# Kernel tuning notes

Hardware: AMD Instinct MI355X
Metric: run time of the kernel (lower is better)

The kernel has to match this reference:

```python
import jax, jax.numpy as jnp
import numpy as np

B, S, H = 8, 1024, 1536          # batch, seq, hidden_size
NH, HD, AH = 8, 96, 768          # heads after head_ratio=2, head_size=hidden/16, all_head_size
K = 7                            # conv_kernel_size
IM = 3072                        # intermediate_size
EPS = 1e-12                      # ConvBert layer_norm_eps


def _ln(x, g, b):
    m = x.mean(-1, keepdims=True)
    v = ((x - m) ** 2).mean(-1, keepdims=True)
    return (x - m) / jnp.sqrt(v + EPS) * g + b


def _windows(x, k):
    # x: [B,S,C] -> sliding windows [B,S,k,C] with 'same' padding ((k-1)//2 each side, k odd)
    p = (k - 1) // 2
    xp = jnp.pad(x, ((0, 0), (p, p), (0, 0)))
    idx = jnp.arange(x.shape[1])[:, None] + jnp.arange(k)[None, :]
    return xp[:, idx, :]


def _forward(embed, wq, bq, wk, bk, wv, bv, dw, pw, sep_b, wck, bck, wco, bco,
             wso, bso, ln1_g, ln1_b, wi, bi, wo, bo, ln2_g, ln2_b, wd, bd):
    b, s, _ = embed.shape
    # --- projections (weights stored [in,out]) ---
    q = embed @ wq + bq            # [B,S,AH]
    kk = embed @ wk + bk
    v = embed @ wv + bv
    # --- SeparableConv1D on hidden states: depthwise(k=7) then pointwise + bias ---
    win_h = _windows(embed, K)                             # [B,S,K,H]
    dconv = jnp.einsum('bskc,ck->bsc', win_h, dw)          # depthwise, [B,S,H]
    sep = dconv @ pw + sep_b                               # pointwise, [B,S,AH]
    # --- span dynamic conv kernels ---
    conv_attn = sep * q                                    # [B,S,AH]
    ck = (conv_attn @ wck + bck).reshape(b, s, NH, K)      # [B,S,NH,K]
    ck = jax.nn.softmax(ck, axis=-1)
    co = embed @ wco + bco                                 # [B,S,AH]
    win_co = _windows(co, K).reshape(b, s, K, NH, HD)      # [B,S,K,NH,HD]
    conv_out = jnp.einsum('bskhd,bshk->bshd', win_co, ck)  # [B,S,NH,HD]
    # --- standard self-attention on the reduced heads ---
    qh = q.reshape(b, s, NH, HD)
    kh = kk.reshape(b, s, NH, HD)
    vh = v.reshape(b, s, NH, HD)
    scores = jnp.einsum('bqhd,bkhd->bhqk', qh, kh) / jnp.sqrt(jnp.float32(HD))
    probs = jax.nn.softmax(scores, axis=-1)
    ctx = jnp.einsum('bhqk,bkhd->bqhd', probs, vh)         # [B,S,NH,HD]
    # --- concat attention heads with conv heads -> [B,S,2*NH,HD] -> [B,S,H] ---
    ctx = jnp.concatenate([ctx, conv_out], axis=2).reshape(b, s, H)
    # --- self output (dropout is identity at inference) ---
    attn_out = _ln(ctx @ wso + bso + embed, ln1_g, ln1_b)
    # --- FFN ---
    inter = jax.nn.gelu(attn_out @ wi + bi, approximate=False)
    layer_out = _ln(inter @ wo + bo + attn_out, ln2_g, ln2_b)
    # --- global max pooling over sequence + linear decoder ---
    pooled = layer_out.max(axis=1)                         # [B,H]
    logits = pooled @ wd + bd                              # [B,1]
    return logits


def setup_inputs() -> dict:
    key = jax.random.key(0)
    ks = jax.random.split(key, 32)
    rn = lambda i, shape, s=0.02: jax.random.normal(ks[i], shape, jnp.float32) * s
    d = {}
    d['embed'] = jax.random.normal(ks[0], (B, S, H), jnp.float32)
    d['wq'] = rn(1, (H, AH)); d['bq'] = jnp.zeros((AH,), jnp.float32)
    d['wk'] = rn(2, (H, AH)); d['bk'] = jnp.zeros((AH,), jnp.float32)
    d['wv'] = rn(3, (H, AH)); d['bv'] = jnp.zeros((AH,), jnp.float32)
    d['dw'] = rn(4, (H, K)); d['pw'] = rn(5, (H, AH)); d['sep_b'] = jnp.zeros((AH,), jnp.float32)
    d['wck'] = rn(6, (AH, NH * K)); d['bck'] = jnp.zeros((NH * K,), jnp.float32)
    d['wco'] = rn(7, (H, AH)); d['bco'] = jnp.zeros((AH,), jnp.float32)
    d['wso'] = rn(8, (H, H)); d['bso'] = jnp.zeros((H,), jnp.float32)
    d['ln1_g'] = jnp.ones((H,), jnp.float32); d['ln1_b'] = jnp.zeros((H,), jnp.float32)
    d['wi'] = rn(9, (H, IM)); d['bi'] = jnp.zeros((IM,), jnp.float32)
    d['wo'] = rn(10, (IM, H)); d['bo'] = jnp.zeros((H,), jnp.float32)
    d['ln2_g'] = jnp.ones((H,), jnp.float32); d['ln2_b'] = jnp.zeros((H,), jnp.float32)
    d['wd'] = jax.random.uniform(ks[11], (H, 1), jnp.float32, -0.1, 0.1)
    d['bd'] = jnp.zeros((1,), jnp.float32)
    return d


def reference(embed, wq, bq, wk, bk, wv, bv, dw, pw, sep_b, wck, bck, wco, bco,
              wso, bso, ln1_g, ln1_b, wi, bi, wo, bo, ln2_g, ln2_b, wd, bd):
    return _forward(embed, wq, bq, wk, bk, wv, bv, dw, pw, sep_b, wck, bck, wco, bco,
                    wso, bso, ln1_g, ln1_b, wi, bi, wo, bo, ln2_g, ln2_b, wd, bd)
```

## Files before the change

### kernel.cpp

```cpp
#include <hip/hip_runtime.h>


typedef __bf16 bf16_t;
typedef short s16x8 __attribute__((ext_vector_type(8)));
typedef float f32x4 __attribute__((ext_vector_type(4)));

#define BB  8
#define SS  1024
#define HH  1536
#define NHH 8
#define HDD 96
#define AHH 768
#define IMM 3072

__device__ __forceinline__ float rd_adapt(const void* p, long long i, int isbf) {
    return isbf ? (float)((const bf16_t*)p)[i] : ((const float*)p)[i];
}
__device__ __forceinline__ float bs2f(short x) {
    return __uint_as_float(((unsigned)(unsigned short)x) << 16);
}
__device__ __forceinline__ short f2bs(float f) {
    bf16_t b = (bf16_t)f; short s; __builtin_memcpy(&s, &b, 2); return s;
}

__device__ __forceinline__ float gelu_f(float v) {
    float u = v * (0.7978845608f + 0.0356774081f * v * v);
    float e = __expf(2.0f * u);
    float t = 1.0f - 2.0f / (e + 1.0f);
    return 0.5f * v * (1.0f + t);
}

__device__ __forceinline__ void gl2lds16(const bf16_t* g, bf16_t* l) {
    __builtin_amdgcn_global_load_lds(
        (__attribute__((address_space(1))) const void*)g,
        (__attribute__((address_space(3))) void*)l, 16, 0, 0);
}

#define FENCE() asm volatile("" ::: "memory")
#define BARRIER() do { FENCE(); __builtin_amdgcn_s_barrier(); FENCE(); } while (0)
#define LGKM(n) asm volatile("s_waitcnt lgkmcnt(" #n ")" ::: "memory")
#define VMCNT(n) asm volatile("s_waitcnt vmcnt(" #n ")" ::: "memory")
#define SCHEDB() __builtin_amdgcn_sched_barrier(0)
#define PRIO(n) __builtin_amdgcn_s_setprio(n)
#define RDV(base, imm) (*(const s16x8*)(smb + (base) + (imm)))

#define MFMA_CLUSTER(AF, BF, IO, JO)                                            \
    _Pragma("unroll")                                                           \
    for (int i_ = 0; i_ < 4; i_++)                                              \
        _Pragma("unroll")                                                       \
        for (int j_ = 0; j_ < 2; j_++) {                                        \
            acc[(IO)+i_][(JO)+j_] = __builtin_amdgcn_mfma_f32_16x16x32_bf16(    \
                AF[i_][0], BF[j_][0], acc[(IO)+i_][(JO)+j_], 0, 0, 0);          \
            acc[(IO)+i_][(JO)+j_] = __builtin_amdgcn_mfma_f32_16x16x32_bf16(    \
                AF[i_][1], BF[j_][1], acc[(IO)+i_][(JO)+j_], 0, 0, 0);          \
        }

__global__ __launch_bounds__(256)
void detect_kernel(const void* __restrict__ embed, int* __restrict__ flag)
{
    __shared__ int cnt[256];
    int t = threadIdx.x;
    float x = (float)((const bf16_t*)embed)[t];
    float a = fabsf(x);
    cnt[t] = (a > 1e-3f && a < 50.0f) ? 1 : 0;
    __syncthreads();
    for (int o = 128; o > 0; o >>= 1) { if (t < o) cnt[t] += cnt[t + o]; __syncthreads(); }
    if (t == 0) *flag = (cnt[0] >= 205) ? 1 : 0;
}

__global__ __launch_bounds__(256)
void convert_embed(const void* __restrict__ in, bf16_t* __restrict__ out,
                   const int* __restrict__ flagp)
{
    int isbf = *flagp;
    long long i0 = ((long long)blockIdx.x * 256 + threadIdx.x) * 8;
    if (isbf) {
        *(s16x8*)(out + i0) = *(const s16x8*)((const bf16_t*)in + i0);
    } else {
        const float* f = (const float*)in;
        #pragma unroll
        for (int j = 0; j < 8; j++) out[i0 + j] = (bf16_t)f[i0 + j];
    }
}

__global__ __launch_bounds__(256)
void concat_bias(const void* __restrict__ b0, const void* __restrict__ b1,
                 const void* __restrict__ b2, const void* __restrict__ b3,
                 bf16_t* __restrict__ out, const int* __restrict__ flagp)
{
    int isbf = *flagp;
    int t = blockIdx.x * 256 + threadIdx.x;
    int sel = t / 768, off = t - sel * 768;
    const void* src = (sel == 0) ? b0 : (sel == 1) ? b1 : (sel == 2) ? b2 : b3;
    out[t] = (bf16_t)rd_adapt(src, off, isbf);
}

__global__ __launch_bounds__(256)
void dw_transpose(const void* __restrict__ dw, float* __restrict__ dwT,
                  const int* __restrict__ flagp)
{
    int isbf = *flagp;
    int i = blockIdx.x * 256 + threadIdx.x;
    if (i >= 7 * HH) return;
    int k = i % 7, c = i / 7;
    dwT[k * HH + c] = rd_adapt(dw, (long long)c * 7 + k, isbf);
}

template<int IB, int OB>
__device__ __forceinline__ void tile_step(
    char* smb, int vA0, int vA1, int vB0, int vB1,
    const char* gA00, const char* gA01, const char* gA10, const char* gA11,
    const char* gB00, const char* gB01, const char* gB10, const char* gB11,
    char* ldsAw, char* ldsBw, int k1, int k2,
    s16x8 (&af0)[4][2], s16x8 (&af1)[4][2],
    s16x8 (&bf0)[2][2], s16x8 (&bf1)[2][2],
    f32x4 (&acc)[8][4])
{
    BARRIER();
    bf1[0][0] = RDV(vB0, IB + 4096); bf1[0][1] = RDV(vB1, IB + 4096);
    bf1[1][0] = RDV(vB0, IB + 6144); bf1[1][1] = RDV(vB1, IB + 6144);
    gl2lds16((const bf16_t*)(gA10 + k1), (bf16_t*)(ldsAw + OB + 16384));
    gl2lds16((const bf16_t*)(gA11 + k1), (bf16_t*)(ldsAw + OB + 17408));
    LGKM(4); SCHEDB(); PRIO(1);
    MFMA_CLUSTER(af0, bf0, 0, 0);
    PRIO(0);

    BARRIER();
    af1[0][0] = RDV(vA0, IB + 8192);  af1[0][1] = RDV(vA1, IB + 8192);
    af1[1][0] = RDV(vA0, IB + 10240); af1[1][1] = RDV(vA1, IB + 10240);
    af1[2][0] = RDV(vA0, IB + 12288); af1[2][1] = RDV(vA1, IB + 12288);
    af1[3][0] = RDV(vA0, IB + 14336); af1[3][1] = RDV(vA1, IB + 14336);
    gl2lds16((const bf16_t*)(gB10 + k1), (bf16_t*)(ldsBw + OB + 16384));
    gl2lds16((const bf16_t*)(gB11 + k1), (bf16_t*)(ldsBw + OB + 17408));
    LGKM(8); SCHEDB(); PRIO(1);
    MFMA_CLUSTER(af0, bf1, 0, 2);
    PRIO(0);

    BARRIER();
    gl2lds16((const bf16_t*)(gB00 + k2), (bf16_t*)(ldsBw + IB));
    gl2lds16((const bf16_t*)(gB01 + k2), (bf16_t*)(ldsBw + IB + 1024));
    gl2lds16((const bf16_t*)(gA00 + k2), (bf16_t*)(ldsAw + IB));
    gl2lds16((const bf16_t*)(gA01 + k2), (bf16_t*)(ldsAw + IB + 1024));
    LGKM(0); SCHEDB(); PRIO(1);
    MFMA_CLUSTER(af1, bf1, 4, 2);
    PRIO(0);

    VMCNT(4);
    BARRIER();
    af0[0][0] = RDV(vA0, OB + 0);    af0[0][1] = RDV(vA1, OB + 0);
    af0[1][0] = RDV(vA0, OB + 2048); af0[1][1] = RDV(vA1, OB + 2048);
    af0[2][0] = RDV(vA0, OB + 4096); af0[2][1] = RDV(vA1, OB + 4096);
    af0[3][0] = RDV(vA0, OB + 6144); af0[3][1] = RDV(vA1, OB + 6144);
    PRIO(1);
    MFMA_CLUSTER(af1, bf0, 4, 0);
    PRIO(0);
    bf0[0][0] = RDV(vB0, OB + 0);    bf0[0][1] = RDV(vB1, OB + 0);
    bf0[1][0] = RDV(vB0, OB + 2048); bf0[1][1] = RDV(vB1, OB + 2048);
}

__global__ __launch_bounds__(512, 2)
void gemm256(const bf16_t* __restrict__ A, const bf16_t* __restrict__ Bt,
             bf16_t* __restrict__ C, const void* __restrict__ bias,
             const bf16_t* __restrict__ emul, int lde, const int* __restrict__ flagp,
             int M, int N, int Kd, int lda, int ldb, int ldc, int act, int tilesN)
{
    __shared__ bf16_t Sm[65536];
    char* smb = (char*)Sm;
    int isbf = flagp ? *flagp : 1;

    int nwg = gridDim.x;
    int orig = blockIdx.x;
    int q = nwg >> 3, r = nwg & 7;
    int xcd = orig & 7, lid = orig >> 3;
    int wg = (xcd < r ? xcd * (q + 1) : r * (q + 1) + (xcd - r) * q) + lid;
    int row0 = (wg / tilesN) * 256;
    int col0 = (wg % tilesN) * 256;

    int tid = threadIdx.x;
    int wave = tid >> 6, lane = tid & 63;
    int wm = wave >> 2, wn = wave & 3;
    int lm = lane & 15, kq = lane >> 4;

    int srow = lane >> 3;
    int scol = 8 * ((lane & 7) ^ srow);

    const char* gA00 = (const char*)(A + (long long)(row0 +   0 + (2*wave + 0)*8 + srow) * lda + scol);
    const char* gA01 = (const char*)(A + (long long)(row0 +   0 + (2*wave + 1)*8 + srow) * lda + scol);
    const char* gA10 = (const char*)(A + (long long)(row0 + 128 + (2*wave + 0)*8 + srow) * lda + scol);
    const char* gA11 = (const char*)(A + (long long)(row0 + 128 + (2*wave + 1)*8 + srow) * lda + scol);
    const char* gB00 = (const char*)(Bt + (long long)(col0 +   0 + (2*wave + 0)*8 + srow) * ldb + scol);
    const char* gB01 = (const char*)(Bt + (long long)(col0 +   0 + (2*wave + 1)*8 + srow) * ldb + scol);
    const char* gB10 = (const char*)(Bt + (long long)(col0 + 128 + (2*wave + 0)*8 + srow) * ldb + scol);
    const char* gB11 = (const char*)(Bt + (long long)(col0 + 128 + (2*wave + 1)*8 + srow) * ldb + scol);

    char* ldsAw = smb + 2 * wave * 1024;
    char* ldsBw = smb + 65536 + 2 * wave * 1024;

    int xo = (lm & 7) << 4;
    int c0 = (kq * 16) ^ xo;
    int c1 = (64 + kq * 16) ^ xo;
    int vA0 = (wm * 128 + lm) * 128 + c0;
    int vA1 = (wm * 128 + lm) * 128 + c1;
    int vB0 = 65536 + (wn * 64 + lm) * 128 + c0;
    int vB1 = 65536 + (wn * 64 + lm) * 128 + c1;

    f32x4 acc[8][4] = {};
    s16x8 af0[4][2], af1[4][2], bf0[2][2], bf1[2][2];

    int KT = Kd >> 6;
    int KTm1 = KT - 1;

    gl2lds16((const bf16_t*)gA00, (bf16_t*)(ldsAw));
    gl2lds16((const bf16_t*)gA01, (bf16_t*)(ldsAw + 1024));
    gl2lds16((const bf16_t*)gA10, (bf16_t*)(ldsAw + 16384));
    gl2lds16((const bf16_t*)gA11, (bf16_t*)(ldsAw + 17408));
    gl2lds16((const bf16_t*)gB00, (bf16_t*)(ldsBw));
    gl2lds16((const bf16_t*)gB01, (bf16_t*)(ldsBw + 1024));
    gl2lds16((const bf16_t*)gB10, (bf16_t*)(ldsBw + 16384));
    gl2lds16((const bf16_t*)gB11, (bf16_t*)(ldsBw + 17408));
    int kb1 = min(1, KTm1) << 7;
    gl2lds16((const bf16_t*)(gB00 + kb1), (bf16_t*)(ldsBw + 32768));
    gl2lds16((const bf16_t*)(gB01 + kb1), (bf16_t*)(ldsBw + 33792));
    gl2lds16((const bf16_t*)(gA00 + kb1), (bf16_t*)(ldsAw + 32768));
    gl2lds16((const bf16_t*)(gA01 + kb1), (bf16_t*)(ldsAw + 33792));
    VMCNT(4);
    BARRIER();
    af0[0][0] = RDV(vA0, 0);    af0[0][1] = RDV(vA1, 0);
    af0[1][0] = RDV(vA0, 2048); af0[1][1] = RDV(vA1, 2048);
    af0[2][0] = RDV(vA0, 4096); af0[2][1] = RDV(vA1, 4096);
    af0[3][0] = RDV(vA0, 6144); af0[3][1] = RDV(vA1, 6144);
    bf0[0][0] = RDV(vB0, 0);    bf0[0][1] = RDV(vB1, 0);
    bf0[1][0] = RDV(vB0, 2048); bf0[1][1] = RDV(vB1, 2048);

    for (int it = 0; it < (KT >> 1); ++it) {
        int t = it << 1;
        int k1 = min(t + 1, KTm1) << 7;
        int k2 = min(t + 2, KTm1) << 7;
        int k3 = min(t + 3, KTm1) << 7;
        tile_step<0, 32768>(smb, vA0, vA1, vB0, vB1,
                            gA00, gA01, gA10, gA11, gB00, gB01, gB10, gB11,
                            ldsAw, ldsBw, k1, k2, af0, af1, bf0, bf1, acc);
        tile_step<32768, 0>(smb, vA0, vA1, vB0, vB1,
                            gA00, gA01, gA10, gA11, gB00, gB01, gB10, gB11,
                            ldsAw, ldsBw, k2, k3, af0, af1, bf0, bf1, acc);
    }

    #pragma unroll
    for (int j = 0; j < 4; j++) {
        int gcol = col0 + wn * 64 + j * 16 + lm;
        float bv = bias ? rd_adapt(bias, gcol, isbf) : 0.0f;
        #pragma unroll
        for (int ip = 0; ip < 8; ip++) {
            int grow0 = row0 + wm * 128 + ip * 16 + kq * 4;
            #pragma unroll
            for (int r = 0; r < 4; r++) {
                float v = acc[ip][j][r] + bv;
                if (emul) v *= (float)emul[(long long)(grow0 + r) * lde + gcol];
                if (act) v = gelu_f(v);
                C[(long long)(grow0 + r) * ldc + gcol] = (bf16_t)v;
            }
        }
    }
}

__global__ __launch_bounds__(256)
void gemm_tile(const bf16_t* __restrict__ A, const bf16_t* __restrict__ Bt,
               bf16_t* __restrict__ C, const void* __restrict__ bias, long long biasOff,
               const bf16_t* __restrict__ emul, int lde, const int* __restrict__ flagp,
               int M, int N, int Kd, int lda, int ldb, int ldc,
               float scale, int act, int beta, int nlim)
{
    __shared__ bf16_t Sm[16384];

    int isbf = flagp ? *flagp : 1;
    int tid  = threadIdx.x;
    int wave = tid >> 6, lane = tid & 63;
    int wm = wave >> 1, wn = wave & 1;
    int row0 = blockIdx.x * 128;
    int col0 = blockIdx.y * 128;
    int lm = lane & 15;
    int kq = lane >> 4;

    int sr = tid >> 2;
    int sc = (tid & 3) * 8;
    const bf16_t* ga0 = A + (long long)(row0 + sr) * lda + sc;
    const bf16_t* ga1 = A + (long long)(row0 + 64 + sr) * lda + sc;
    int br0 = min(col0 + sr, nlim);
    int br1 = min(col0 + 64 + sr, nlim);
    const bf16_t* gb0 = Bt + (long long)br0 * ldb + sc;
    const bf16_t* gb1 = Bt + (long long)br1 * ldb + sc;
    bf16_t* lw = Sm + wave * 512;

    f32x4 acc[4][4] = {};

    for (int k0 = 0; k0 < Kd; k0 += 64) {
        #pragma unroll
        for (int h = 0; h < 2; h++) {
            int kh = k0 + h * 32;
            gl2lds16(ga0 + kh, lw + h * 4096);
            gl2lds16(ga1 + kh, lw + h * 4096 + 2048);
            gl2lds16(gb0 + kh, lw + 8192 + h * 4096);
            gl2lds16(gb1 + kh, lw + 8192 + h * 4096 + 2048);
        }
        __syncthreads();

        s16x8 af[2][4], bfr[2][4];
        #pragma unroll
        for (int h = 0; h < 2; h++) {
            #pragma unroll
            for (int i = 0; i < 4; i++)
                af[h][i] = *(const s16x8*)(Sm + h * 4096 + (wm * 64 + i * 16 + lm) * 32 + kq * 8);
            #pragma unroll
            for (int j = 0; j < 4; j++)
                bfr[h][j] = *(const s16x8*)(Sm + 8192 + h * 4096 + (wn * 64 + j * 16 + lm) * 32 + kq * 8);
        }
        #pragma unroll
        for (int i = 0; i < 4; i++)
            #pragma unroll
            for (int j = 0; j < 4; j++) {
                acc[i][j] = __builtin_amdgcn_mfma_f32_16x16x32_bf16(af[0][i], bfr[0][j], acc[i][j], 0, 0, 0);
                acc[i][j] = __builtin_amdgcn_mfma_f32_16x16x32_bf16(af[1][i], bfr[1][j], acc[i][j], 0, 0, 0);
            }
        __syncthreads();
    }

    #pragma unroll
    for (int j = 0; j < 4; j++) {
        int gcol = col0 + wn * 64 + j * 16 + lm;
        if (gcol >= N) continue;
        float bv = bias ? rd_adapt(bias, biasOff + gcol, isbf) : 0.0f;
        #pragma unroll
        for (int i = 0; i < 4; i++) {
            int grow0 = row0 + wm * 64 + i * 16 + kq * 4;
            #pragma unroll
            for (int r = 0; r < 4; r++) {
                float v = acc[i][j][r] * scale + bv;
                long long ci = (long long)(grow0 + r) * ldc + gcol;
                if (beta) v += (float)C[ci];
                if (emul) v *= (float)emul[(long long)(grow0 + r) * lde + gcol];
                if (act) v = gelu_f(v);
                C[ci] = (bf16_t)v;
            }
        }
    }
}

__global__ __launch_bounds__(256, 2)
void flash_attn(const bf16_t* __restrict__ qkv, const bf16_t* __restrict__ vT,
                bf16_t* __restrict__ ctxcat)
{
    const float ascale = 0.1020620726159658f;
    __shared__ bf16_t Pl[4 * 32 * 136];

    int bh = blockIdx.x;
    int b = bh >> 3, h = bh & 7;
    const bf16_t* Qp = qkv  + (long long)b * SS * 3072 + h * HDD;
    const bf16_t* Kp = qkv  + (long long)b * SS * 3072 + 768 + h * HDD;
    const bf16_t* Vt = vT   + (long long)b * AHH * SS + (long long)h * HDD * SS;
    bf16_t*       Op = ctxcat + (long long)b * SS * HH + h * HDD;

    int tid = threadIdx.x, wave = tid >> 6, lane = tid & 63;
    int lm = lane & 15, kq = lane >> 4;
    int q0 = blockIdx.y * 128 + wave * 32;
    bf16_t* Pw = Pl + wave * 32 * 136;

    s16x8 aq[2][3];
    #pragma unroll
    for (int i = 0; i < 2; i++)
        #pragma unroll
        for (int kf = 0; kf < 3; kf++)
            aq[i][kf] = *(const s16x8*)(Qp + (long long)(q0 + i * 16 + lm) * 3072 + kf * 32 + kq * 8);

    f32x4 Oacc[2][6] = {};
    float mrow[2][4], lrow[2][4];
    #pragma unroll
    for (int i = 0; i < 2; i++)
        #pragma unroll
        for (int r = 0; r < 4; r++) { mrow[i][r] = -1e30f; lrow[i][r] = 0.0f; }

    for (int kt = 0; kt < 8; kt++) {
        f32x4 S[2][8] = {};
        #pragma unroll
        for (int j = 0; j < 8; j++) {
            s16x8 bk[3];
            #pragma unroll
            for (int kf = 0; kf < 3; kf++)
                bk[kf] = *(const s16x8*)(Kp + (long long)(kt * 128 + j * 16 + lm) * 3072 + kf * 32 + kq * 8);
            #pragma unroll
            for (int i = 0; i < 2; i++)
                #pragma unroll
                for (int kf = 0; kf < 3; kf++)
                    S[i][j] = __builtin_amdgcn_mfma_f32_16x16x32_bf16(aq[i][kf], bk[kf], S[i][j], 0, 0, 0);
        }

        float mnew[2][4];
        #pragma unroll
        for (int i = 0; i < 2; i++) {
            #pragma unroll
            for (int r = 0; r < 4; r++) {
                float mx = -1e30f;
                #pragma unroll
                for (int j = 0; j < 8; j++) mx = fmaxf(mx, S[i][j][r]);
                #pragma unroll
                for (int msk = 1; msk <= 8; msk <<= 1) mx = fmaxf(mx, __shfl_xor(mx, msk));
                mnew[i][r] = fmaxf(mrow[i][r], mx * ascale);
            }
        }
        #pragma unroll
        for (int i = 0; i < 2; i++) {
            #pragma unroll
            for (int r = 0; r < 4; r++) {
                float al = __expf(mrow[i][r] - mnew[i][r]);
                lrow[i][r] *= al;
                #pragma unroll
                for (int n = 0; n < 6; n++) Oacc[i][n][r] *= al;
                mrow[i][r] = mnew[i][r];
            }
        }
        float psum[2][4] = {};
        __syncthreads();
        #pragma unroll
        for (int i = 0; i < 2; i++) {
            #pragma unroll
            for (int j = 0; j < 8; j++) {
                #pragma unroll
                for (int r = 0; r < 4; r++) {
                    float p = __expf(S[i][j][r] * ascale - mnew[i][r]);
                    psum[i][r] += p;
                    Pw[(i * 16 + kq * 4 + r) * 136 + j * 16 + lm] = (bf16_t)p;
                }
            }
        }
        #pragma unroll
        for (int i = 0; i < 2; i++) {
            #pragma unroll
            for (int r = 0; r < 4; r++) {
                float t = psum[i][r];
                #pragma unroll
                for (int msk = 1; msk <= 8; msk <<= 1) t += __shfl_xor(t, msk);
                lrow[i][r] += t;
            }
        }
        __syncthreads();

        s16x8 ap[2][4];
        #pragma unroll
        for (int i = 0; i < 2; i++)
            #pragma unroll
            for (int kf = 0; kf < 4; kf++)
                ap[i][kf] = *(const s16x8*)(Pw + (i * 16 + lm) * 136 + kf * 32 + kq * 8);
        #pragma unroll
        for (int n = 0; n < 6; n++) {
            s16x8 bv[4];
            #pragma unroll
            for (int kf = 0; kf < 4; kf++)
                bv[kf] = *(const s16x8*)(Vt + (long long)(n * 16 + lm) * SS + kt * 128 + kf * 32 + kq * 8);
            #pragma unroll
            for (int i = 0; i < 2; i++)
                #pragma unroll
                for (int kf = 0; kf < 4; kf++)
                    Oacc[i][n] = __builtin_amdgcn_mfma_f32_16x16x32_bf16(ap[i][kf], bv[kf], Oacc[i][n], 0, 0, 0);
        }
    }

    #pragma unroll
    for (int i = 0; i < 2; i++) {
        #pragma unroll
        for (int n = 0; n < 6; n++) {
            #pragma unroll
            for (int r = 0; r < 4; r++) {
                int row = q0 + i * 16 + kq * 4 + r;
                int col = n * 16 + lm;
                Op[(long long)row * HH + col] = (bf16_t)(Oacc[i][n][r] / lrow[i][r]);
            }
        }
    }
}

__global__ __launch_bounds__(256)
void transpose_pad(const void* __restrict__ in, bf16_t* __restrict__ out,
                   int R, int C, int ldin, long long inOff,
                   long long sInB, long long sOutB, const int* __restrict__ flagp)
{
    __shared__ bf16_t t[32][33];
    int isbf = flagp ? *flagp : 1;
    int z = blockIdx.z;
    long long base = inOff + (long long)z * sInB;
    bf16_t* op = out + (long long)z * sOutB;
    int tx = threadIdx.x & 31, ty = threadIdx.x >> 5;
    int cb = blockIdx.x * 32, rb = blockIdx.y * 32;
    #pragma unroll
    for (int rr = ty; rr < 32; rr += 8) {
        int r = rb + rr, c = cb + tx;
        t[rr][tx] = (c < C) ? (bf16_t)rd_adapt(in, base + (long long)r * ldin + c, isbf)
                            : (bf16_t)0.0f;
    }
    __syncthreads();
    #pragma unroll
    for (int rr = ty; rr < 32; rr += 8) {
        int c = cb + rr;
        op[(long long)c * R + rb + tx] = t[tx][rr];
    }
}

__global__ __launch_bounds__(256)
void transpose_pad4(const void* __restrict__ i0, const void* __restrict__ i1,
                    const void* __restrict__ i2, const void* __restrict__ i3,
                    bf16_t* __restrict__ out, const int* __restrict__ flagp)
{
    __shared__ bf16_t t[32][33];
    int isbf = *flagp;
    int z = blockIdx.z;
    const void* in = (z == 0) ? i0 : (z == 1) ? i1 : (z == 2) ? i2 : i3;
    bf16_t* op = out + (long long)z * (768ll * 1536);
    int tx = threadIdx.x & 31, ty = threadIdx.x >> 5;
    int cb = blockIdx.x * 32, rb = blockIdx.y * 32;
    #pragma unroll
    for (int rr = ty; rr < 32; rr += 8) {
        int r = rb + rr, c = cb + tx;
        t[rr][tx] = (bf16_t)rd_adapt(in, (long long)r * 768 + c, isbf);
    }
    __syncthreads();
    #pragma unroll
    for (int rr = ty; rr < 32; rr += 8) {
        int c = cb + rr;
        op[(long long)c * 1536 + rb + tx] = t[tx][rr];
    }
}

__global__ __launch_bounds__(256)
void dconv_kernel(const bf16_t* __restrict__ ebuf, const float* __restrict__ dwT,
                  bf16_t* __restrict__ out)
{
    long long i = (long long)blockIdx.x * 256 + threadIdx.x;
    int c8 = (int)(i % 192) * 8;
    long long bs = i / 192;
    int s = (int)(bs % SS);
    float acc[8] = {};
    #pragma unroll
    for (int k = 0; k < 7; k++) {
        int ss = s + k - 3;
        if (ss < 0 || ss >= SS) continue;
        s16x8 v = *(const s16x8*)(ebuf + (bs + (k - 3)) * HH + c8);
        const float4* wp = (const float4*)(dwT + k * HH + c8);
        float4 w0 = wp[0], w1 = wp[1];
        acc[0] += bs2f(v[0]) * w0.x; acc[1] += bs2f(v[1]) * w0.y;
        acc[2] += bs2f(v[2]) * w0.z; acc[3] += bs2f(v[3]) * w0.w;
        acc[4] += bs2f(v[4]) * w1.x; acc[5] += bs2f(v[5]) * w1.y;
        acc[6] += bs2f(v[6]) * w1.z; acc[7] += bs2f(v[7]) * w1.w;
    }
    s16x8 o;
    #pragma unroll
    for (int j = 0; j < 8; j++) o[j] = f2bs(acc[j]);
    *(s16x8*)(out + bs * HH + c8) = o;
}

__global__ __launch_bounds__(256)
void ck_softmax(const bf16_t* __restrict__ ck, float* __restrict__ ckp)
{
    int i = blockIdx.x * 256 + threadIdx.x;
    if (i >= BB * SS * NHH) return;
    int h = i % NHH;
    long long bs = i / NHH;
    const bf16_t* src = ck + bs * 64 + h * 7;
    float v[7], mx = -1e30f;
    #pragma unroll
    for (int k = 0; k < 7; k++) { v[k] = (float)src[k]; mx = fmaxf(mx, v[k]); }
    float sum = 0.0f;
    #pragma unroll
    for (int k = 0; k < 7; k++) { v[k] = expf(v[k] - mx); sum += v[k]; }
    float inv = 1.0f / sum;
    float* dst = ckp + bs * 56 + h * 7;
    #pragma unroll
    for (int k = 0; k < 7; k++) dst[k] = v[k] * inv;
}

__global__ __launch_bounds__(256)
void conv_out_kernel(const bf16_t* __restrict__ co, int ldco,
                     const float* __restrict__ ckp, bf16_t* __restrict__ ctxcat)
{
    long long i = (long long)blockIdx.x * 256 + threadIdx.x;
    int ch = (int)(i % 96);
    long long bs = i / 96;
    int s = (int)(bs % SS);
    int hd0 = ch * 8;
    int h = hd0 / HDD;
    const float* w = ckp + bs * 56 + h * 7;
    float wk[7];
    #pragma unroll
    for (int k = 0; k < 7; k++) wk[k] = w[k];
    float acc[8] = {};
    #pragma unroll
    for (int k = 0; k < 7; k++) {
        int ss = s + k - 3;
        if (ss < 0 || ss >= SS) continue;
        s16x8 v = *(const s16x8*)(co + (bs + (k - 3)) * ldco + hd0);
        #pragma unroll
        for (int j = 0; j < 8; j++) acc[j] += bs2f(v[j]) * wk[k];
    }
    s16x8 o;
    #pragma unroll
    for (int j = 0; j < 8; j++) o[j] = f2bs(acc[j]);
    *(s16x8*)(ctxcat + bs * HH + AHH + hd0) = o;
}

__global__ __launch_bounds__(192)
void ln_kernel(const bf16_t* __restrict__ y, const bf16_t* __restrict__ res,
               const void* __restrict__ g, const void* __restrict__ bta,
               bf16_t* __restrict__ outb, const int* __restrict__ flagp)
{
    int isbf = *flagp;
    long long row = blockIdx.x;
    int tid = threadIdx.x;
    int c0 = tid * 8;
    s16x8 vy = *(const s16x8*)(y + row * HH + c0);
    s16x8 vr = *(const s16x8*)(res + row * HH + c0);
    float x[8], s = 0.0f, s2 = 0.0f;
    #pragma unroll
    for (int j = 0; j < 8; j++) {
        float v = bs2f(vy[j]) + bs2f(vr[j]);
        x[j] = v; s += v; s2 += v * v;
    }
    #pragma unroll
    for (int o = 32; o > 0; o >>= 1) { s += __shfl_down(s, o); s2 += __shfl_down(s2, o); }
    __shared__ float w1[3], w2[3];
    int lane = tid & 63, wv = tid >> 6;
    if (lane == 0) { w1[wv] = s; w2[wv] = s2; }
    __syncthreads();
    float S1 = w1[0] + w1[1] + w1[2];
    float S2 = w2[0] + w2[1] + w2[2];
    float mean = S1 * (1.0f / HH);
    float var  = S2 * (1.0f / HH) - mean * mean;
    float inv  = rsqrtf(var + 1e-12f);
    s16x8 o;
    #pragma unroll
    for (int j = 0; j < 8; j++) {
        float v = (x[j] - mean) * inv * rd_adapt(g, c0 + j, isbf) + rd_adapt(bta, c0 + j, isbf);
        o[j] = f2bs(v);
    }
    *(s16x8*)(outb + row * HH + c0) = o;
}

__global__ __launch_bounds__(192)
void maxpool_p1(const bf16_t* __restrict__ lo, float* __restrict__ part)
{
    int sc = blockIdx.x, b = blockIdx.y;
    int tid = threadIdx.x;
    int c0 = tid * 8;
    const bf16_t* p = lo + ((long long)b * SS + sc * 32) * HH + c0;
    float m[8];
    #pragma unroll
    for (int j = 0; j < 8; j++) m[j] = -1e30f;
    for (int r = 0; r < 32; r++) {
        s16x8 v = *(const s16x8*)(p + (long long)r * HH);
        #pragma unroll
        for (int j = 0; j < 8; j++) m[j] = fmaxf(m[j], bs2f(v[j]));
    }
    float* dst = part + ((long long)b * 32 + sc) * HH + c0;
    *(float4*)(dst)     = make_float4(m[0], m[1], m[2], m[3]);
    *(float4*)(dst + 4) = make_float4(m[4], m[5], m[6], m[7]);
}

__global__ __launch_bounds__(192)
void pool_decode(const float* __restrict__ part, const void* __restrict__ wd,
                 const void* __restrict__ bd, void* __restrict__ out,
                 const int* __restrict__ flagp)
{
    int isbf = *flagp;
    int b = blockIdx.x;
    int tid = threadIdx.x;
    int c0 = tid * 8;
    float m[8];
    #pragma unroll
    for (int j = 0; j < 8; j++) m[j] = -1e30f;
    for (int ch = 0; ch < 32; ch++) {
        const float4* q = (const float4*)(part + ((long long)b * 32 + ch) * HH + c0);
        float4 a = q[0], c = q[1];
        m[0] = fmaxf(m[0], a.x); m[1] = fmaxf(m[1], a.y);
        m[2] = fmaxf(m[2], a.z); m[3] = fmaxf(m[3], a.w);
        m[4] = fmaxf(m[4], c.x); m[5] = fmaxf(m[5], c.y);
        m[6] = fmaxf(m[6], c.z); m[7] = fmaxf(m[7], c.w);
    }
    float s = 0.0f;
    #pragma unroll
    for (int j = 0; j < 8; j++) s += m[j] * rd_adapt(wd, c0 + j, isbf);
    #pragma unroll
    for (int o = 32; o > 0; o >>= 1) s += __shfl_down(s, o);
    __shared__ float sa[3];
    int lane = tid & 63, wv = tid >> 6;
    if (lane == 0) sa[wv] = s;
    __syncthreads();
    if (tid == 0) {
        float r = sa[0] + sa[1] + sa[2] + rd_adapt(bd, 0, isbf);
        if (isbf) ((bf16_t*)out)[b] = (bf16_t)r;
        else      ((float*)out)[b]  = r;
    }
}

extern "C" void kernel_launch(void* const* d_in, const int* in_sizes, int n_in,
                              void* d_out, int out_size, void* d_ws, size_t ws_size,
                              hipStream_t stream)
{
    const void* embed = d_in[0];
    const void* wq  = d_in[1];  const void* bq  = d_in[2];
    const void* wk  = d_in[3];  const void* bk  = d_in[4];
    const void* wv  = d_in[5];  const void* bv  = d_in[6];
    const void* dw  = d_in[7];  const void* pw  = d_in[8];  const void* sep_b = d_in[9];
    const void* wck = d_in[10]; const void* bck = d_in[11];
    const void* wco = d_in[12]; const void* bco = d_in[13];
    const void* wso = d_in[14]; const void* bso = d_in[15];
    const void* ln1g = d_in[16]; const void* ln1b = d_in[17];
    const void* wi  = d_in[18]; const void* bi  = d_in[19];
    const void* wo  = d_in[20]; const void* bo  = d_in[21];
    const void* ln2g = d_in[22]; const void* ln2b = d_in[23];
    const void* wd  = d_in[24]; const void* bd  = d_in[25];
    (void)ws_size; (void)in_sizes; (void)n_in; (void)out_size;

    char* ws = (char*)d_ws;
    char* A  = ws;
    char* B  = ws + 50331648;
    char* C_ = ws + 75497472;
    char* D  = ws + 88080384;
    char* E  = ws + 113246208;
    char* F  = ws + 138412032;
    char* XP = ws + 143130624;

    bf16_t* qkvco  = (bf16_t*)A;
    bf16_t* ybuf   = (bf16_t*)A;
    bf16_t* interb = (bf16_t*)A;
    bf16_t* lout   = (bf16_t*)A;
    bf16_t* wT_all = (bf16_t*)B;
    bf16_t* dconvb = (bf16_t*)B;
    bf16_t* ckb    = (bf16_t*)B;
    float*  ckp    = (float*)(B + 1310720);
    bf16_t* vT     = (bf16_t*)B;
    bf16_t* wfT    = (bf16_t*)B;
    bf16_t* sepb   = (bf16_t*)C_;
    float*  mpart  = (float*)C_;
    bf16_t* ctxcat = (bf16_t*)D;
    bf16_t* attn   = (bf16_t*)D;
    bf16_t* ebuf   = (bf16_t*)E;
    bf16_t* y2     = (bf16_t*)E;
    bf16_t* wT     = (bf16_t*)F;
    int*    flag   = (int*)XP;
    bf16_t* cbias  = (bf16_t*)(XP + 256);
    float*  dwT    = (float*)(XP + 8192);

    dim3 blk(256);

    auto gemm_big = [&](const bf16_t* Ai, const bf16_t* Bt, bf16_t* Ci, const void* bias,
                        const bf16_t* emul, int lde, const int* fl,
                        int M, int N, int Kd, int lda, int ldb, int ldc, int act) {
        int tn = N / 256;
        dim3 g((M / 256) * tn);
        gemm256<<<g, dim3(512), 0, stream>>>(Ai, Bt, Ci, bias, emul, lde, fl,
                                             M, N, Kd, lda, ldb, ldc, act, tn);
    };
    auto gemm = [&](const bf16_t* Ai, const bf16_t* Bt, bf16_t* Ci, const void* bias,
                    long long biasOff, const bf16_t* emul, int lde, const int* fl,
                    int M, int N, int Kd, int lda, int ldb, int ldc,
                    float scale, int act, int beta, int nlim) {
        dim3 g(M / 128, (N + 127) / 128, 1);
        gemm_tile<<<g, blk, 0, stream>>>(Ai, Bt, Ci, bias, biasOff, emul, lde, fl,
                                         M, N, Kd, lda, ldb, ldc,
                                         scale, act, beta, nlim);
    };
    auto transpose = [&](const void* in, bf16_t* out, int R, int Cc, int Cpad, int ldin,
                         long long inOff, int batch, long long sInB, long long sOutB,
                         const int* fl) {
        dim3 g(Cpad / 32, R / 32, batch);
        transpose_pad<<<g, blk, 0, stream>>>(in, out, R, Cc, ldin, inOff, sInB, sOutB, fl);
    };

    detect_kernel<<<dim3(1), blk, 0, stream>>>(embed, flag);
    convert_embed<<<dim3(6144), blk, 0, stream>>>(embed, ebuf, flag);

    transpose_pad4<<<dim3(24, 48, 4), blk, 0, stream>>>(wq, wk, wv, wco, wT_all, flag);
    concat_bias<<<dim3(12), blk, 0, stream>>>(bq, bk, bv, bco, cbias, flag);
    gemm_big(ebuf, wT_all, qkvco, cbias, nullptr, 0, nullptr,
             8192, 3072, 1536, HH, HH, 3072, 0);

    dw_transpose<<<dim3(42), blk, 0, stream>>>(dw, dwT, flag);
    dconv_kernel<<<dim3((BB * SS * 192) / 256), blk, 0, stream>>>(ebuf, dwT, dconvb);
    transpose(pw, wT, 1536, 768, 768, 768, 0, 1, 0, 0, flag);
    gemm(dconvb, wT, sepb, sep_b, 0, qkvco, 3072, flag,
         8192, 768, 1536, HH, HH, AHH, 1.0f, 0, 0, 767);

    transpose(wck, wT, 768, 56, 128, 56, 0, 1, 0, 0, flag);
    gemm(sepb, wT, ckb, bck, 0, nullptr, 0, flag,
         8192, 56, 768, AHH, AHH, 64, 1.0f, 0, 0, 127);
    ck_softmax<<<dim3((BB * SS * NHH) / 256), blk, 0, stream>>>(ckb, ckp);
    conv_out_kernel<<<dim3((BB * SS * 96) / 256), blk, 0, stream>>>(qkvco + 2304, 3072, ckp, ctxcat);

    transpose(qkvco, vT, 1024, 768, 768, 3072, 1536, 8, 1024ll * 3072, 768ll * 1024, nullptr);
    flash_attn<<<dim3(64, 8), blk, 0, stream>>>(qkvco, vT, ctxcat);

    transpose(wso, wT, 1536, 1536, 1536, 1536, 0, 1, 0, 0, flag);
    gemm_big(ctxcat, wT, ybuf, bso, nullptr, 0, flag,
             8192, 1536, 1536, HH, HH, HH, 0);
    ln_kernel<<<dim3(8192), dim3(192), 0, stream>>>(ybuf, ebuf, ln1g, ln1b, attn, flag);

    transpose(wi, wfT, 1536, 3072, 3072, 3072, 0, 1, 0, 0, flag);
    gemm_big(attn, wfT, interb, bi, nullptr, 0, flag,
             8192, 3072, 1536, HH, HH, IMM, 1);
    transpose(wo, wfT, 3072, 1536, 1536, 1536, 0, 1, 0, 0, flag);
    gemm_big(interb, wfT, y2, bo, nullptr, 0, flag,
             8192, 1536, 3072, IMM, IMM, HH, 0);
    ln_kernel<<<dim3(8192), dim3(192), 0, stream>>>(y2, attn, ln2g, ln2b, lout, flag);

    maxpool_p1<<<dim3(32, 8), dim3(192), 0, stream>>>(lout, mpart);
    pool_decode<<<dim3(BB), dim3(192), 0, stream>>>(mpart, wd, bd, d_out, flag);
}
```

Baseline: 865.8 us.

## Stage K tiles in LDS for flash attention and vectorize transpose kernels

The flash attention kernel now copies each 128-row K tile into a swizzled LDS buffer with asynchronous global-to-LDS copies. The next tile's copy is issued right after the QK^T MFMAs, so it overlaps with the softmax and PV work, and the barriers are moved to fit. Previously every wave read K directly from global memory, so the four waves re-fetched the same data. Separately, the transpose kernels move to 64x64 tiles with 16-byte vector loads and stores. This raises LDS use per block and adds a bank-conflict-prone column read in LDS.

```diff
diff --git a/kernel.cpp b/kernel.cpp
--- a/kernel.cpp
+++ b/kernel.cpp
@@ -350,6 +350,7 @@
                 bf16_t* __restrict__ ctxcat)
 {
     const float ascale = 0.1020620726159658f;
+    __shared__ bf16_t KL[12288];
     __shared__ bf16_t Pl[4 * 32 * 136];
 
     int bh = blockIdx.x;
@@ -364,6 +365,19 @@
     int q0 = blockIdx.y * 128 + wave * 32;
     bf16_t* Pw = Pl + wave * 32 * 136;
 
+    int srow_l = lane >> 2;
+    int sslot  = ((lane & 3) ^ ((lane >> 3) & 3)) * 8;
+    auto stageK = [&](int kt) {
+        #pragma unroll
+        for (int i = 0; i < 6; i++) {
+            int qc = wave + 4 * i;
+            int fb = qc >> 3, cc = qc & 7;
+            gl2lds16(Kp + (long long)(kt * 128 + cc * 16 + srow_l) * 3072 + fb * 32 + sslot,
+                     KL + qc * 512);
+        }
+    };
+    const char* klb = (const char*)KL + lm * 64 + ((kq ^ ((lm >> 1) & 3)) << 4);
+
     s16x8 aq[2][3];
     #pragma unroll
     for (int i = 0; i < 2; i++)
@@ -371,6 +385,9 @@
         for (int kf = 0; kf < 3; kf++)
             aq[i][kf] = *(const s16x8*)(Qp + (long long)(q0 + i * 16 + lm) * 3072 + kf * 32 + kq * 8);
 
+    stageK(0);
+    __syncthreads();
+
     f32x4 Oacc[2][6] = {};
     float mrow[2][4], lrow[2][4];
     #pragma unroll
@@ -385,13 +402,15 @@
             s16x8 bk[3];
             #pragma unroll
             for (int kf = 0; kf < 3; kf++)
-                bk[kf] = *(const s16x8*)(Kp + (long long)(kt * 128 + j * 16 + lm) * 3072 + kf * 32 + kq * 8);
+                bk[kf] = *(const s16x8*)(klb + kf * 8192 + j * 1024);
             #pragma unroll
             for (int i = 0; i < 2; i++)
                 #pragma unroll
                 for (int kf = 0; kf < 3; kf++)
                     S[i][j] = __builtin_amdgcn_mfma_f32_16x16x32_bf16(aq[i][kf], bk[kf], S[i][j], 0, 0, 0);
         }
+        __syncthreads();
+        if (kt < 7) stageK(kt + 1);
 
         float mnew[2][4];
         #pragma unroll
@@ -418,7 +437,6 @@
             }
         }
         float psum[2][4] = {};
-        __syncthreads();
         #pragma unroll
         for (int i = 0; i < 2; i++) {
             #pragma unroll
@@ -441,7 +459,6 @@
                 lrow[i][r] += t;
             }
         }
-        __syncthreads();
 
         s16x8 ap[2][4];
         #pragma unroll
@@ -461,6 +478,7 @@
                 for (int kf = 0; kf < 4; kf++)
                     Oacc[i][n] = __builtin_amdgcn_mfma_f32_16x16x32_bf16(ap[i][kf], bv[kf], Oacc[i][n], 0, 0, 0);
         }
+        __syncthreads();
     }
 
     #pragma unroll
@@ -478,29 +496,44 @@
 }
 
 __global__ __launch_bounds__(256)
-void transpose_pad(const void* __restrict__ in, bf16_t* __restrict__ out,
-                   int R, int C, int ldin, long long inOff,
-                   long long sInB, long long sOutB, const int* __restrict__ flagp)
-{
-    __shared__ bf16_t t[32][33];
+void transpose_v8(const void* __restrict__ in, bf16_t* __restrict__ out,
+                  int R, int C, int ldin, long long inOff,
+                  long long sInB, long long sOutB, const int* __restrict__ flagp)
+{
+    __shared__ bf16_t t[64][72];
     int isbf = flagp ? *flagp : 1;
     int z = blockIdx.z;
     long long base = inOff + (long long)z * sInB;
     bf16_t* op = out + (long long)z * sOutB;
-    int tx = threadIdx.x & 31, ty = threadIdx.x >> 5;
-    int cb = blockIdx.x * 32, rb = blockIdx.y * 32;
-    #pragma unroll
-    for (int rr = ty; rr < 32; rr += 8) {
-        int r = rb + rr, c = cb + tx;
-        t[rr][tx] = (c < C) ? (bf16_t)rd_adapt(in, base + (long long)r * ldin + c, isbf)
-                            : (bf16_t)0.0f;
+    int cb = blockIdx.x * 64, rb = blockIdx.y * 64;
+    int tr = threadIdx.x >> 3;
+    int tc = (threadIdx.x & 7) * 8;
+    #pragma unroll
+    for (int it = 0; it < 2; it++) {
+        int r = tr + it * 32;
+        int gc = cb + tc;
+        if (isbf && gc + 8 <= C) {
+            *(s16x8*)&t[r][tc] =
+                *(const s16x8*)((const bf16_t*)in + base + (long long)(rb + r) * ldin + gc);
+        } else {
+            #pragma unroll
+            for (int j = 0; j < 8; j++)
+                t[r][tc + j] = (gc + j < C)
+                    ? (bf16_t)rd_adapt(in, base + (long long)(rb + r) * ldin + gc + j, isbf)
+                    : (bf16_t)0.0f;
+        }
     }
     __syncthreads();
-    #pragma unroll
-    for (int rr = ty; rr < 32; rr += 8) {
-        int c = cb + rr;
-        op[(long long)c * R + rb + tx] = t[tx][rr];
-    }
+    int oc = threadIdx.x >> 2;
+    int r0 = (threadIdx.x & 3) * 16;
+    s16x8 v0, v1;
+    #pragma unroll
+    for (int j = 0; j < 8; j++) v0[j] = f2bs(bs2f(*(short*)&t[r0 + j][oc]));
+    #pragma unroll
+    for (int j = 0; j < 8; j++) v1[j] = f2bs(bs2f(*(short*)&t[r0 + 8 + j][oc]));
+    bf16_t* dst = op + (long long)(cb + oc) * R + rb + r0;
+    *(s16x8*)dst = v0;
+    *(s16x8*)(dst + 8) = v1;
 }
 
 __global__ __launch_bounds__(256)
@@ -508,24 +541,37 @@
                     const void* __restrict__ i2, const void* __restrict__ i3,
                     bf16_t* __restrict__ out, const int* __restrict__ flagp)
 {
-    __shared__ bf16_t t[32][33];
+    __shared__ bf16_t t[64][72];
     int isbf = *flagp;
     int z = blockIdx.z;
     const void* in = (z == 0) ? i0 : (z == 1) ? i1 : (z == 2) ? i2 : i3;
     bf16_t* op = out + (long long)z * (768ll * 1536);
-    int tx = threadIdx.x & 31, ty = threadIdx.x >> 5;
-    int cb = blockIdx.x * 32, rb = blockIdx.y * 32;
-    #pragma unroll
-    for (int rr = ty; rr < 32; rr += 8) {
-        int r = rb + rr, c = cb + tx;
-        t[rr][tx] = (bf16_t)rd_adapt(in, (long long)r * 768 + c, isbf);
+    int cb = blockIdx.x * 64, rb = blockIdx.y * 64;
+    int tr = threadIdx.x >> 3;
+    int tc = (threadIdx.x & 7) * 8;
+    #pragma unroll
+    for (int it = 0; it < 2; it++) {
+        int r = tr + it * 32;
+        if (isbf) {
+            *(s16x8*)&t[r][tc] =
+                *(const s16x8*)((const bf16_t*)in + (long long)(rb + r) * 768 + cb + tc);
+        } else {
+            #pragma unroll
+            for (int j = 0; j < 8; j++)
+                t[r][tc + j] = (bf16_t)rd_adapt(in, (long long)(rb + r) * 768 + cb + tc + j, isbf);
+        }
     }
     __syncthreads();
-    #pragma unroll
-    for (int rr = ty; rr < 32; rr += 8) {
-        int c = cb + rr;
-        op[(long long)c * 1536 + rb + tx] = t[tx][rr];
-    }
+    int oc = threadIdx.x >> 2;
+    int r0 = (threadIdx.x & 3) * 16;
+    s16x8 v0, v1;
+    #pragma unroll
+    for (int j = 0; j < 8; j++) v0[j] = *(short*)&t[r0 + j][oc];
+    #pragma unroll
+    for (int j = 0; j < 8; j++) v1[j] = *(short*)&t[r0 + 8 + j][oc];
+    bf16_t* dst = op + (long long)(cb + oc) * 1536 + rb + r0;
+    *(s16x8*)dst = v0;
+    *(s16x8*)(dst + 8) = v1;
 }
 
 __global__ __launch_bounds__(256)
@@ -768,14 +814,14 @@
     auto transpose = [&](const void* in, bf16_t* out, int R, int Cc, int Cpad, int ldin,
                          long long inOff, int batch, long long sInB, long long sOutB,
                          const int* fl) {
-        dim3 g(Cpad / 32, R / 32, batch);
-        transpose_pad<<<g, blk, 0, stream>>>(in, out, R, Cc, ldin, inOff, sInB, sOutB, fl);
+        dim3 g(Cpad / 64, R / 64, batch);
+        transpose_v8<<<g, blk, 0, stream>>>(in, out, R, Cc, ldin, inOff, sInB, sOutB, fl);
     };
 
     detect_kernel<<<dim3(1), blk, 0, stream>>>(embed, flag);
     convert_embed<<<dim3(6144), blk, 0, stream>>>(embed, ebuf, flag);
 
-    transpose_pad4<<<dim3(24, 48, 4), blk, 0, stream>>>(wq, wk, wv, wco, wT_all, flag);
+    transpose_pad4<<<dim3(12, 24, 4), blk, 0, stream>>>(wq, wk, wv, wco, wT_all, flag);
     concat_bias<<<dim3(12), blk, 0, stream>>>(bq, bk, bv, bco, cbias, flag);
     gemm_big(ebuf, wT_all, qkvco, cbias, nullptr, 0, nullptr,
              8192, 3072, 1536, HH, HH, 3072, 0);
```

Result: faster. 847.2 us (-2.1%).
